# Kernel tuning notes

Measured on AMD Instinct MI355X. Metric: run time of the kernel, lower is better.

## Reference

```python
import jax, jax.numpy as jnp
import numpy as np

B, FEAT, HID, LAT, NQ, NEMB = 2048, 840, 256, 128, 12, 512


def setup_inputs() -> dict:
    key = jax.random.key(0)
    ks = jax.random.split(key, 6)
    return {
        "x": jax.random.normal(ks[0], (B, FEAT), jnp.float32),
        "w1": jax.random.normal(ks[1], (HID, 1, 3), jnp.float32) * 0.1,   # Conv1d(1->256, k=3)
        "b1": jnp.zeros((HID,), jnp.float32),
        "w2": jax.random.normal(ks[2], (LAT, HID, 3), jnp.float32) * 0.05,  # Conv1d(256->128, k=3)
        "b2": jnp.zeros((LAT,), jnp.float32),
        # 12 codebooks of (512, 128), init uniform(-1/n_emb, 1/n_emb) per the torch code
        "codebooks": jax.random.uniform(ks[3], (NQ, NEMB, LAT), jnp.float32, -1.0 / NEMB, 1.0 / NEMB),
    }


def _encode(x, w1, b1, w2, b2):
    # x: (B, FEAT) -> unsqueeze channel dim -> NCW conv stack -> adaptive avg pool(1)
    h = x[:, None, :]  # (B, 1, FEAT)
    h = jax.lax.conv_general_dilated(h, w1, (1,), 'SAME',
                                     dimension_numbers=('NCH', 'OIH', 'NCH'))
    h = jax.nn.relu(h + b1[None, :, None])
    h = jax.lax.conv_general_dilated(h, w2, (1,), 'SAME',
                                     dimension_numbers=('NCH', 'OIH', 'NCH'))
    h = jax.nn.relu(h + b2[None, :, None])
    return h.mean(axis=2)  # AdaptiveAvgPool1d(1) + squeeze -> (B, LAT)


def _rvq(z_flat, codebooks):
    # sequential residual VQ: 12 stages of cdist -> argmin -> gather -> residual update
    def step(residual, cb):
        # squared L2 distances: ||r||^2 - 2 r C^T + ||c||^2, shape (B, NEMB)
        d = (jnp.sum(residual ** 2, axis=1, keepdims=True)
             - 2.0 * (residual @ cb.T)
             + jnp.sum(cb ** 2, axis=1)[None, :])
        idx = jnp.argmin(d, axis=1)          # (B,)
        q = cb[idx]                          # (B, LAT) embedding gather
        residual = residual - jax.lax.stop_gradient(q)  # .detach() in torch
        return residual, (q, idx)

    _, (qs, idxs) = jax.lax.scan(step, z_flat, codebooks)  # qs: (NQ, B, LAT)
    return qs.sum(axis=0), idxs.T  # (B, LAT), (B, NQ)


def reference(x, w1, b1, w2, b2, codebooks):
    z = _encode(x, w1, b1, w2, b2)            # (B, LAT)
    zq, idx = _rvq(z, codebooks)              # L = 1 so flat == (B, LAT)
    return zq[:, None, :], idx[:, None, :]    # (B, 1, LAT), (B, 1, NQ)
```

## Files before the change

### kernel.cpp

```cpp
#include <hip/hip_runtime.h>

#define B_SZ 2048
#define FEAT 840
#define HID  256
#define LAT  128
#define NQ   12
#define NEMB 512

#define T_SUB 40
#define HSTR  43
#define H2STR 41

__device__ __forceinline__ float np8_combine(const float* r) {
    float sA = __fadd_rn(r[0], r[1]);
    float sB = __fadd_rn(r[2], r[3]);
    float sC = __fadd_rn(r[4], r[5]);
    float sD = __fadd_rn(r[6], r[7]);
    return __fadd_rn(__fadd_rn(sA, sB), __fadd_rn(sC, sD));
}

__global__ __launch_bounds__(256) void w2r_kernel(const float* __restrict__ w2,
                                                  float* __restrict__ w2r)
{
    int p = blockIdx.x * 256 + threadIdx.x;
    if (p >= HID * 384) return;
    int c2 = p / 384, r = p - c2 * 384;
    int ly = r / 12, jk = r - ly * 12;
    int j = jk / 3, k = jk - j * 3;
    w2r[p] = w2[(size_t)(ly*4 + j)*768 + c2*3 + k];
}

#define CSTEP(A0, A1, A2, H0, H1, H2, H3, H4, H5, H6)                  \
    {                                                                  \
        sk[0][0][0] = __fmaf_rn(A0.x, H0, sk[0][0][0]);                \
        sk[0][0][1] = __fmaf_rn(A0.y, H1, sk[0][0][1]);                \
        sk[0][0][2] = __fmaf_rn(A0.z, H2, sk[0][0][2]);                \
        sk[0][1][0] = __fmaf_rn(A0.x, H1, sk[0][1][0]);                \
        sk[0][1][1] = __fmaf_rn(A0.y, H2, sk[0][1][1]);                \
        sk[0][1][2] = __fmaf_rn(A0.z, H3, sk[0][1][2]);                \
        sk[0][2][0] = __fmaf_rn(A0.x, H2, sk[0][2][0]);                \
        sk[0][2][1] = __fmaf_rn(A0.y, H3, sk[0][2][1]);                \
        sk[0][2][2] = __fmaf_rn(A0.z, H4, sk[0][2][2]);                \
        sk[0][3][0] = __fmaf_rn(A0.x, H3, sk[0][3][0]);                \
        sk[0][3][1] = __fmaf_rn(A0.y, H4, sk[0][3][1]);                \
        sk[0][3][2] = __fmaf_rn(A0.z, H5, sk[0][3][2]);                \
        sk[0][4][0] = __fmaf_rn(A0.x, H4, sk[0][4][0]);                \
        sk[0][4][1] = __fmaf_rn(A0.y, H5, sk[0][4][1]);                \
        sk[0][4][2] = __fmaf_rn(A0.z, H6, sk[0][4][2]);                \
        sk[1][0][0] = __fmaf_rn(A0.w, H0, sk[1][0][0]);                \
        sk[1][0][1] = __fmaf_rn(A1.x, H1, sk[1][0][1]);                \
        sk[1][0][2] = __fmaf_rn(A1.y, H2, sk[1][0][2]);                \
        sk[1][1][0] = __fmaf_rn(A0.w, H1, sk[1][1][0]);                \
        sk[1][1][1] = __fmaf_rn(A1.x, H2, sk[1][1][1]);                \
        sk[1][1][2] = __fmaf_rn(A1.y, H3, sk[1][1][2]);                \
        sk[1][2][0] = __fmaf_rn(A0.w, H2, sk[1][2][0]);                \
        sk[1][2][1] = __fmaf_rn(A1.x, H3, sk[1][2][1]);                \
        sk[1][2][2] = __fmaf_rn(A1.y, H4, sk[1][2][2]);                \
        sk[1][3][0] = __fmaf_rn(A0.w, H3, sk[1][3][0]);                \
        sk[1][3][1] = __fmaf_rn(A1.x, H4, sk[1][3][1]);                \
        sk[1][3][2] = __fmaf_rn(A1.y, H5, sk[1][3][2]);                \
        sk[1][4][0] = __fmaf_rn(A0.w, H4, sk[1][4][0]);                \
        sk[1][4][1] = __fmaf_rn(A1.x, H5, sk[1][4][1]);                \
        sk[1][4][2] = __fmaf_rn(A1.y, H6, sk[1][4][2]);                \
        sk[2][0][0] = __fmaf_rn(A1.z, H0, sk[2][0][0]);                \
        sk[2][0][1] = __fmaf_rn(A1.w, H1, sk[2][0][1]);                \
        sk[2][0][2] = __fmaf_rn(A2.x, H2, sk[2][0][2]);                \
        sk[2][1][0] = __fmaf_rn(A1.z, H1, sk[2][1][0]);                \
        sk[2][1][1] = __fmaf_rn(A1.w, H2, sk[2][1][1]);                \
        sk[2][1][2] = __fmaf_rn(A2.x, H3, sk[2][1][2]);                \
        sk[2][2][0] = __fmaf_rn(A1.z, H2, sk[2][2][0]);                \
        sk[2][2][1] = __fmaf_rn(A1.w, H3, sk[2][2][1]);                \
        sk[2][2][2] = __fmaf_rn(A2.x, H4, sk[2][2][2]);                \
        sk[2][3][0] = __fmaf_rn(A1.z, H3, sk[2][3][0]);                \
        sk[2][3][1] = __fmaf_rn(A1.w, H4, sk[2][3][1]);                \
        sk[2][3][2] = __fmaf_rn(A2.x, H5, sk[2][3][2]);                \
        sk[2][4][0] = __fmaf_rn(A1.z, H4, sk[2][4][0]);                \
        sk[2][4][1] = __fmaf_rn(A1.w, H5, sk[2][4][1]);                \
        sk[2][4][2] = __fmaf_rn(A2.x, H6, sk[2][4][2]);                \
        sk[3][0][0] = __fmaf_rn(A2.y, H0, sk[3][0][0]);                \
        sk[3][0][1] = __fmaf_rn(A2.z, H1, sk[3][0][1]);                \
        sk[3][0][2] = __fmaf_rn(A2.w, H2, sk[3][0][2]);                \
        sk[3][1][0] = __fmaf_rn(A2.y, H1, sk[3][1][0]);                \
        sk[3][1][1] = __fmaf_rn(A2.z, H2, sk[3][1][1]);                \
        sk[3][1][2] = __fmaf_rn(A2.w, H3, sk[3][1][2]);                \
        sk[3][2][0] = __fmaf_rn(A2.y, H2, sk[3][2][0]);                \
        sk[3][2][1] = __fmaf_rn(A2.z, H3, sk[3][2][1]);                \
        sk[3][2][2] = __fmaf_rn(A2.w, H4, sk[3][2][2]);                \
        sk[3][3][0] = __fmaf_rn(A2.y, H3, sk[3][3][0]);                \
        sk[3][3][1] = __fmaf_rn(A2.z, H4, sk[3][3][1]);                \
        sk[3][3][2] = __fmaf_rn(A2.w, H5, sk[3][3][2]);                \
        sk[3][4][0] = __fmaf_rn(A2.y, H4, sk[3][4][0]);                \
        sk[3][4][1] = __fmaf_rn(A2.z, H5, sk[3][4][1]);                \
        sk[3][4][2] = __fmaf_rn(A2.w, H6, sk[3][4][2]);                \
    }

template <int USE_WR>
__global__ __launch_bounds__(256) void enc32_kernel(
    const float* __restrict__ x,  const float* __restrict__ w1,
    const float* __restrict__ b1, const float* __restrict__ w2,
    const float* __restrict__ w2r,
    const float* __restrict__ b2, float* __restrict__ zout)
{
    __shared__ float xp[FEAT + 4];
    __shared__ float h1s[HID * HSTR];
    __shared__ float leafs[LAT * 8];

    const int tid = threadIdx.x;
    const int b   = blockIdx.x;
    const int tx  = tid & 7;
    const int ly  = tid >> 3;
    const int u0  = tx * 5;

    const float wA = w1[tid*3+0], wB = w1[tid*3+1], wC = w1[tid*3+2];
    const float b1c = b1[tid];
    float b2v[4];
#pragma unroll
    for (int j = 0; j < 4; ++j) b2v[j] = b2[ly*4 + j];

    for (int i = tid; i < FEAT + 2; i += 256)
        xp[i] = (i >= 1 && i <= FEAT) ? x[(size_t)b*FEAT + i - 1] : 0.f;

    float racc[8];
    int leaf_id = 0, leaf_pos = 0;
#pragma unroll
    for (int j = 0; j < 8; ++j) racc[j] = 0.f;

    __syncthreads();
    for (int t0 = 0; t0 < FEAT; t0 += T_SUB) {
        const bool edge = (t0 == 0) | (t0 + T_SUB == FEAT);
        if (edge) {
            for (int tp = 0; tp < T_SUB + 2; ++tp) {
                int tg = t0 - 1 + tp;
                float v = 0.f;
                if (tg >= 0 && tg < FEAT) {
                    float s = __fadd_rn(__fadd_rn(__fmul_rn(wA, xp[tg]),
                                                  __fmul_rn(wB, xp[tg+1])),
                                        __fmul_rn(wC, xp[tg+2]));
                    s = __fadd_rn(s, b1c);
                    v = s > 0.f ? s : 0.f;
                }
                h1s[tid*HSTR + tp] = v;
            }
        } else {
#pragma unroll 2
            for (int tp = 0; tp < T_SUB + 2; ++tp) {
                int tg = t0 - 1 + tp;
                float s = __fadd_rn(__fadd_rn(__fmul_rn(wA, xp[tg]),
                                              __fmul_rn(wB, xp[tg+1])),
                                    __fmul_rn(wC, xp[tg+2]));
                s = __fadd_rn(s, b1c);
                h1s[tid*HSTR + tp] = s > 0.f ? s : 0.f;
            }
        }
        __syncthreads();

        float sk[4][5][3];
#pragma unroll
        for (int j = 0; j < 4; ++j)
#pragma unroll
            for (int i = 0; i < 5; ++i)
#pragma unroll
                for (int k = 0; k < 3; ++k) sk[j][i][k] = 0.f;

        if (USE_WR) {
            const float* __restrict__ wbase = w2r + ly*12;
            const float* __restrict__ hbase = &h1s[u0];

            float4 cA0, cA1, cA2, cB0, cB1, cB2;
            float  hA0, hA1, hA2, hA3, hA4, hA5, hA6;
            float  hB0, hB1, hB2, hB3, hB4, hB5, hB6;

            {
                const float4* pa = (const float4*)(wbase);
                const float4* pb = (const float4*)(wbase + 384);
                cA0 = pa[0]; cA1 = pa[1]; cA2 = pa[2];
                cB0 = pb[0]; cB1 = pb[1]; cB2 = pb[2];
                hA0 = hbase[0]; hA1 = hbase[1]; hA2 = hbase[2];
                hA3 = hbase[3]; hA4 = hbase[4]; hA5 = hbase[5]; hA6 = hbase[6];
                const float* hbB = hbase + HSTR;
                hB0 = hbB[0]; hB1 = hbB[1]; hB2 = hbB[2];
                hB3 = hbB[3]; hB4 = hbB[4]; hB5 = hbB[5]; hB6 = hbB[6];
            }

#pragma unroll 2
            for (int p = 0; p < HID/2 - 1; ++p) {
                const float* wn = wbase + (size_t)(p + 1) * 768;
                const float4* pa = (const float4*)(wn);
                const float4* pb = (const float4*)(wn + 384);
                float4 nA0 = pa[0], nA1 = pa[1], nA2 = pa[2];
                float4 nB0 = pb[0], nB1 = pb[1], nB2 = pb[2];
                const float* hn = hbase + (size_t)(p + 1) * 2 * HSTR;
                float nhA0 = hn[0], nhA1 = hn[1], nhA2 = hn[2], nhA3 = hn[3],
                      nhA4 = hn[4], nhA5 = hn[5], nhA6 = hn[6];
                const float* hnB = hn + HSTR;
                float nhB0 = hnB[0], nhB1 = hnB[1], nhB2 = hnB[2], nhB3 = hnB[3],
                      nhB4 = hnB[4], nhB5 = hnB[5], nhB6 = hnB[6];

                CSTEP(cA0, cA1, cA2, hA0, hA1, hA2, hA3, hA4, hA5, hA6)
                CSTEP(cB0, cB1, cB2, hB0, hB1, hB2, hB3, hB4, hB5, hB6)

                cA0 = nA0; cA1 = nA1; cA2 = nA2;
                cB0 = nB0; cB1 = nB1; cB2 = nB2;
                hA0 = nhA0; hA1 = nhA1; hA2 = nhA2; hA3 = nhA3;
                hA4 = nhA4; hA5 = nhA5; hA6 = nhA6;
                hB0 = nhB0; hB1 = nhB1; hB2 = nhB2; hB3 = nhB3;
                hB4 = nhB4; hB5 = nhB5; hB6 = nhB6;
            }
            CSTEP(cA0, cA1, cA2, hA0, hA1, hA2, hA3, hA4, hA5, hA6)
            CSTEP(cB0, cB1, cB2, hB0, hB1, hB2, hB3, hB4, hB5, hB6)
        } else {
            const float* __restrict__ wp = w2 + (size_t)(ly*4)*768;
            for (int c2 = 0; c2 < HID; ++c2) {
                const float* hp = &h1s[c2*HSTR + u0];
                float hv[7];
#pragma unroll
                for (int m = 0; m < 7; ++m) hv[m] = hp[m];
#pragma unroll
                for (int j = 0; j < 4; ++j) {
                    float wa = wp[j*768 + c2*3 + 0];
                    float wb = wp[j*768 + c2*3 + 1];
                    float wc = wp[j*768 + c2*3 + 2];
#pragma unroll
                    for (int i = 0; i < 5; ++i) {
                        sk[j][i][0] = __fmaf_rn(wa, hv[i],   sk[j][i][0]);
                        sk[j][i][1] = __fmaf_rn(wb, hv[i+1], sk[j][i][1]);
                        sk[j][i][2] = __fmaf_rn(wc, hv[i+2], sk[j][i][2]);
                    }
                }
            }
        }
        __syncthreads();

#pragma unroll
        for (int j = 0; j < 4; ++j)
#pragma unroll
            for (int i = 0; i < 5; ++i) {
                float hh = __fadd_rn(__fadd_rn(sk[j][i][0], sk[j][i][1]), sk[j][i][2]);
                hh = __fadd_rn(hh, b2v[j]);
                hh = hh > 0.f ? hh : 0.f;
                h1s[(ly*4 + j)*H2STR + u0 + i] = hh;
            }
        __syncthreads();

        if (tid < LAT) {
            for (int tt = 0; tt < T_SUB; ++tt) {
                float v = h1s[tid*H2STR + tt];
                int j = leaf_pos & 7;
                racc[j] = (leaf_pos < 8) ? v : __fadd_rn(racc[j], v);
                ++leaf_pos;
                int llen = (leaf_id == 7) ? 112 : 104;
                if (leaf_pos == llen) {
                    leafs[tid*8 + leaf_id] = np8_combine(racc);
                    ++leaf_id; leaf_pos = 0;
                }
            }
        }
        __syncthreads();
    }

    if (tid < LAT) {
        const float* L = &leafs[tid*8];
        float s0 = __fadd_rn(L[0], L[1]);
        float s1 = __fadd_rn(L[2], L[3]);
        float sA = __fadd_rn(s0, s1);
        float s2 = __fadd_rn(L[4], L[5]);
        float s3 = __fadd_rn(L[6], L[7]);
        float sB = __fadd_rn(s2, s3);
        float tot = __fadd_rn(sA, sB);
        zout[(size_t)b*LAT + tid] = __fdiv_rn(tot, 840.0f);
    }
}

__global__ __launch_bounds__(256) void rvq32_kernel(
    const float* __restrict__ cb, const float* __restrict__ z,
    float* __restrict__ zqout, float* __restrict__ oidx)
{
    __shared__ float rr[LAT];
    __shared__ float Ash;
    __shared__ float redd[256];
    __shared__ int   rede[256];
    __shared__ float sredd[64];
    __shared__ int   srede[64];
    __shared__ int   beste;
    __shared__ float qv[NQ * LAT];

    const int tid = threadIdx.x;
    const int b   = blockIdx.x;

    if (tid < LAT) rr[tid] = z[(size_t)b*LAT + tid];
    __syncthreads();

    for (int q = 0; q < NQ; ++q) {
        const float* __restrict__ cbq = cb + (size_t)q * NEMB * LAT;

        if (tid == 0) {
            float r8[8];
#pragma unroll
            for (int j = 0; j < 8; ++j) r8[j] = __fmul_rn(rr[j], rr[j]);
            for (int i = 8; i < LAT; i += 8)
#pragma unroll
                for (int j = 0; j < 8; ++j)
                    r8[j] = __fadd_rn(r8[j], __fmul_rn(rr[i+j], rr[i+j]));
            Ash = np8_combine(r8);
        }
        __syncthreads();

        float dmin = 0.f; int emin = 0;
#pragma unroll
        for (int h = 0; h < 2; ++h) {
            int e = 2*tid + h;
            const float* __restrict__ cp = cbq + (size_t)e*LAT;
            float dot = 0.f;
            float c8[8];
#pragma unroll
            for (int j = 0; j < 8; ++j) {
                float c = cp[j];
                c8[j] = __fmul_rn(c, c);
                dot = __fmaf_rn(c, rr[j], dot);
            }
            for (int i = 8; i < LAT; i += 8)
#pragma unroll
                for (int j = 0; j < 8; ++j) {
                    float c = cp[i+j];
                    dot = __fmaf_rn(c, rr[i+j], dot);
                    c8[j] = __fadd_rn(c8[j], __fmul_rn(c, c));
                }
            float cn = np8_combine(c8);
            float G  = __fmul_rn(2.0f, dot);
            float d  = __fadd_rn(__fsub_rn(Ash, G), cn);
            if (h == 0) { dmin = d; emin = e; }
            else if (d < dmin) { dmin = d; emin = e; }
        }
        redd[tid] = dmin; rede[tid] = emin;
        __syncthreads();

        if (tid < 64) {
            float bb = redd[tid*4]; int ee = rede[tid*4];
            for (int j = 1; j < 4; ++j) {
                float dj = redd[tid*4 + j];
                if (dj < bb) { bb = dj; ee = rede[tid*4 + j]; }
            }
            sredd[tid] = bb; srede[tid] = ee;
        }
        __syncthreads();
        if (tid == 0) {
            float bb = sredd[0]; int ee = srede[0];
            for (int j = 1; j < 64; ++j) {
                float dj = sredd[j];
                if (dj < bb) { bb = dj; ee = srede[j]; }
            }
            beste = ee;
            oidx[(size_t)b*NQ + q] = (float)ee;
        }
        __syncthreads();

        if (tid < LAT) {
            float cv = cbq[(size_t)beste*LAT + tid];
            qv[q*LAT + tid] = cv;
            rr[tid] = __fsub_rn(rr[tid], cv);
        }
        __syncthreads();
    }

    if (tid < LAT) {
        float s = qv[tid];
        for (int s2 = 1; s2 < NQ; ++s2)
            s = __fadd_rn(s, qv[s2*LAT + tid]);
        zqout[(size_t)b*LAT + tid] = s;
    }
}

extern "C" void kernel_launch(void* const* d_in, const int* in_sizes, int n_in,
                              void* d_out, int out_size, void* d_ws, size_t ws_size,
                              hipStream_t stream)
{
    (void)in_sizes; (void)n_in; (void)out_size;
    const float* x  = (const float*)d_in[0];
    const float* w1 = (const float*)d_in[1];
    const float* b1 = (const float*)d_in[2];
    const float* w2 = (const float*)d_in[3];
    const float* b2 = (const float*)d_in[4];
    const float* cb = (const float*)d_in[5];

    float* out  = (float*)d_out;
    float* zq   = out;
    float* oidx = out + (size_t)B_SZ * LAT;

    const size_t w2r_bytes = (size_t)HID * 384 * sizeof(float);

    if (ws_size >= w2r_bytes) {
        float* w2r = (float*)d_ws;
        w2r_kernel<<<(HID*384 + 255)/256, 256, 0, stream>>>(w2, w2r);
        enc32_kernel<1><<<B_SZ, 256, 0, stream>>>(x, w1, b1, w2, w2r, b2, zq);
    } else {
        enc32_kernel<0><<<B_SZ, 256, 0, stream>>>(x, w1, b1, w2, nullptr, b2, zq);
    }
    rvq32_kernel<<<B_SZ, 256, 0, stream>>>(cb, zq, zq, oidx);
}
```

Before: 6.231 ms.

## Transpose conv1 activations in LDS and repack w2 into 4-channel chunks

The conv1 output tile in shared memory changes from channel-major with stride 43 to time-major with stride 260, so each thread can read four input channels at once with float4 loads. The w2 repack kernel now groups weights in chunks of 4 input channels per output-row group, and the inner loop handles 4 channels per iteration with 12 float4 weight loads and 7 float4 activation loads. This removes the scalar LDS loads and the manual software prefetch of the previous loop. In exchange it raises register pressure, and the conv1 writes now land at stride 260 with possible bank conflicts.

Measured after the change: 6.553 ms. +5.2%, slower.

```diff
diff --git a/kernel.cpp b/kernel.cpp
--- a/kernel.cpp
+++ b/kernel.cpp
@@ -8,7 +8,8 @@
 #define NEMB 512
 
 #define T_SUB 40
-#define HSTR  43
+#define NU    42
+#define HTSTR 260
 #define H2STR 41
 
 __device__ __forceinline__ float np8_combine(const float* r) {
@@ -19,15 +20,17 @@
     return __fadd_rn(__fadd_rn(sA, sB), __fadd_rn(sC, sD));
 }
 
-__global__ __launch_bounds__(256) void w2r_kernel(const float* __restrict__ w2,
-                                                  float* __restrict__ w2r)
+__global__ __launch_bounds__(256) void w2q_kernel(const float* __restrict__ w2,
+                                                  float* __restrict__ w2q)
 {
-    int p = blockIdx.x * 256 + threadIdx.x;
-    if (p >= HID * 384) return;
-    int c2 = p / 384, r = p - c2 * 384;
-    int ly = r / 12, jk = r - ly * 12;
-    int j = jk / 3, k = jk - j * 3;
-    w2r[p] = w2[(size_t)(ly*4 + j)*768 + c2*3 + k];
+    int o = blockIdx.x * 256 + threadIdx.x;
+    if (o >= HID * 384) return;
+    int ch  = o / 1536, rem = o - ch * 1536;
+    int ly  = rem / 48, s48 = rem - ly * 48;
+    int q   = s48 / 12, jk  = s48 - q * 12;
+    int j   = jk / 3,   k   = jk - j * 3;
+    int c2  = ch * 4 + q;
+    w2q[o] = w2[(size_t)(ly*4 + j)*768 + c2*3 + k];
 }
 
 #define CSTEP(A0, A1, A2, H0, H1, H2, H3, H4, H5, H6)                  \
@@ -94,15 +97,15 @@
         sk[3][4][2] = __fmaf_rn(A2.w, H6, sk[3][4][2]);                \
     }
 
-template <int USE_WR>
+template <int USE_WQ>
 __global__ __launch_bounds__(256) void enc32_kernel(
     const float* __restrict__ x,  const float* __restrict__ w1,
     const float* __restrict__ b1, const float* __restrict__ w2,
-    const float* __restrict__ w2r,
+    const float* __restrict__ w2q,
     const float* __restrict__ b2, float* __restrict__ zout)
 {
     __shared__ float xp[FEAT + 4];
-    __shared__ float h1s[HID * HSTR];
+    __shared__ float h1t[NU * HTSTR];
     __shared__ float leafs[LAT * 8];
 
     const int tid = threadIdx.x;
@@ -128,9 +131,10 @@
     __syncthreads();
     for (int t0 = 0; t0 < FEAT; t0 += T_SUB) {
         const bool edge = (t0 == 0) | (t0 + T_SUB == FEAT);
+        float* hw = &h1t[tid];
         if (edge) {
-            for (int tp = 0; tp < T_SUB + 2; ++tp) {
-                int tg = t0 - 1 + tp;
+            for (int u = 0; u < NU; ++u) {
+                int tg = t0 - 1 + u;
                 float v = 0.f;
                 if (tg >= 0 && tg < FEAT) {
                     float s = __fadd_rn(__fadd_rn(__fmul_rn(wA, xp[tg]),
@@ -139,17 +143,17 @@
                     s = __fadd_rn(s, b1c);
                     v = s > 0.f ? s : 0.f;
                 }
-                h1s[tid*HSTR + tp] = v;
+                hw[u*HTSTR] = v;
             }
         } else {
 #pragma unroll 2
-            for (int tp = 0; tp < T_SUB + 2; ++tp) {
-                int tg = t0 - 1 + tp;
+            for (int u = 0; u < NU; ++u) {
+                int tg = t0 - 1 + u;
                 float s = __fadd_rn(__fadd_rn(__fmul_rn(wA, xp[tg]),
                                               __fmul_rn(wB, xp[tg+1])),
                                     __fmul_rn(wC, xp[tg+2]));
                 s = __fadd_rn(s, b1c);
-                h1s[tid*HSTR + tp] = s > 0.f ? s : 0.f;
+                hw[u*HTSTR] = s > 0.f ? s : 0.f;
             }
         }
         __syncthreads();
@@ -162,59 +166,36 @@
 #pragma unroll
                 for (int k = 0; k < 3; ++k) sk[j][i][k] = 0.f;
 
-        if (USE_WR) {
-            const float* __restrict__ wbase = w2r + ly*12;
-            const float* __restrict__ hbase = &h1s[u0];
-
-            float4 cA0, cA1, cA2, cB0, cB1, cB2;
-            float  hA0, hA1, hA2, hA3, hA4, hA5, hA6;
-            float  hB0, hB1, hB2, hB3, hB4, hB5, hB6;
-
-            {
-                const float4* pa = (const float4*)(wbase);
-                const float4* pb = (const float4*)(wbase + 384);
-                cA0 = pa[0]; cA1 = pa[1]; cA2 = pa[2];
-                cB0 = pb[0]; cB1 = pb[1]; cB2 = pb[2];
-                hA0 = hbase[0]; hA1 = hbase[1]; hA2 = hbase[2];
-                hA3 = hbase[3]; hA4 = hbase[4]; hA5 = hbase[5]; hA6 = hbase[6];
-                const float* hbB = hbase + HSTR;
-                hB0 = hbB[0]; hB1 = hbB[1]; hB2 = hbB[2];
-                hB3 = hbB[3]; hB4 = hbB[4]; hB5 = hbB[5]; hB6 = hbB[6];
-            }
-
+        if (USE_WQ) {
+            const float* __restrict__ hb = &h1t[u0 * HTSTR];
 #pragma unroll 2
-            for (int p = 0; p < HID/2 - 1; ++p) {
-                const float* wn = wbase + (size_t)(p + 1) * 768;
-                const float4* pa = (const float4*)(wn);
-                const float4* pb = (const float4*)(wn + 384);
-                float4 nA0 = pa[0], nA1 = pa[1], nA2 = pa[2];
-                float4 nB0 = pb[0], nB1 = pb[1], nB2 = pb[2];
-                const float* hn = hbase + (size_t)(p + 1) * 2 * HSTR;
-                float nhA0 = hn[0], nhA1 = hn[1], nhA2 = hn[2], nhA3 = hn[3],
-                      nhA4 = hn[4], nhA5 = hn[5], nhA6 = hn[6];
-                const float* hnB = hn + HSTR;
-                float nhB0 = hnB[0], nhB1 = hnB[1], nhB2 = hnB[2], nhB3 = hnB[3],
-                      nhB4 = hnB[4], nhB5 = hnB[5], nhB6 = hnB[6];
-
-                CSTEP(cA0, cA1, cA2, hA0, hA1, hA2, hA3, hA4, hA5, hA6)
-                CSTEP(cB0, cB1, cB2, hB0, hB1, hB2, hB3, hB4, hB5, hB6)
-
-                cA0 = nA0; cA1 = nA1; cA2 = nA2;
-                cB0 = nB0; cB1 = nB1; cB2 = nB2;
-                hA0 = nhA0; hA1 = nhA1; hA2 = nhA2; hA3 = nhA3;
-                hA4 = nhA4; hA5 = nhA5; hA6 = nhA6;
-                hB0 = nhB0; hB1 = nhB1; hB2 = nhB2; hB3 = nhB3;
-                hB4 = nhB4; hB5 = nhB5; hB6 = nhB6;
-            }
-            CSTEP(cA0, cA1, cA2, hA0, hA1, hA2, hA3, hA4, hA5, hA6)
-            CSTEP(cB0, cB1, cB2, hB0, hB1, hB2, hB3, hB4, hB5, hB6)
+            for (int ch = 0; ch < HID/4; ++ch) {
+                const float4* wq = (const float4*)(w2q + ((size_t)ch*32 + ly)*48);
+                float4 q0 = wq[0],  q1 = wq[1],  q2 = wq[2];
+                float4 q3 = wq[3],  q4 = wq[4],  q5 = wq[5];
+                float4 q6 = wq[6],  q7 = wq[7],  q8 = wq[8];
+                float4 q9 = wq[9],  q10 = wq[10], q11 = wq[11];
+                const float4* h0p = (const float4*)(hb + 0*HTSTR + ch*4);
+                const float4* h1p = (const float4*)(hb + 1*HTSTR + ch*4);
+                const float4* h2p = (const float4*)(hb + 2*HTSTR + ch*4);
+                const float4* h3p = (const float4*)(hb + 3*HTSTR + ch*4);
+                const float4* h4p = (const float4*)(hb + 4*HTSTR + ch*4);
+                const float4* h5p = (const float4*)(hb + 5*HTSTR + ch*4);
+                const float4* h6p = (const float4*)(hb + 6*HTSTR + ch*4);
+                float4 m0 = *h0p, m1 = *h1p, m2 = *h2p, m3 = *h3p;
+                float4 m4 = *h4p, m5 = *h5p, m6 = *h6p;
+                CSTEP(q0, q1, q2,  m0.x, m1.x, m2.x, m3.x, m4.x, m5.x, m6.x)
+                CSTEP(q3, q4, q5,  m0.y, m1.y, m2.y, m3.y, m4.y, m5.y, m6.y)
+                CSTEP(q6, q7, q8,  m0.z, m1.z, m2.z, m3.z, m4.z, m5.z, m6.z)
+                CSTEP(q9, q10, q11, m0.w, m1.w, m2.w, m3.w, m4.w, m5.w, m6.w)
+            }
         } else {
             const float* __restrict__ wp = w2 + (size_t)(ly*4)*768;
+            const float* __restrict__ hb = &h1t[u0 * HTSTR];
             for (int c2 = 0; c2 < HID; ++c2) {
-                const float* hp = &h1s[c2*HSTR + u0];
                 float hv[7];
 #pragma unroll
-                for (int m = 0; m < 7; ++m) hv[m] = hp[m];
+                for (int m = 0; m < 7; ++m) hv[m] = hb[m*HTSTR + c2];
 #pragma unroll
                 for (int j = 0; j < 4; ++j) {
                     float wa = wp[j*768 + c2*3 + 0];
@@ -238,13 +219,13 @@
                 float hh = __fadd_rn(__fadd_rn(sk[j][i][0], sk[j][i][1]), sk[j][i][2]);
                 hh = __fadd_rn(hh, b2v[j]);
                 hh = hh > 0.f ? hh : 0.f;
-                h1s[(ly*4 + j)*H2STR + u0 + i] = hh;
+                h1t[(ly*4 + j)*H2STR + u0 + i] = hh;
             }
         __syncthreads();
 
         if (tid < LAT) {
             for (int tt = 0; tt < T_SUB; ++tt) {
-                float v = h1s[tid*H2STR + tt];
+                float v = h1t[tid*H2STR + tt];
                 int j = leaf_pos & 7;
                 racc[j] = (leaf_pos < 8) ? v : __fadd_rn(racc[j], v);
                 ++leaf_pos;
@@ -386,12 +367,12 @@
     float* zq   = out;
     float* oidx = out + (size_t)B_SZ * LAT;
 
-    const size_t w2r_bytes = (size_t)HID * 384 * sizeof(float);
-
-    if (ws_size >= w2r_bytes) {
-        float* w2r = (float*)d_ws;
-        w2r_kernel<<<(HID*384 + 255)/256, 256, 0, stream>>>(w2, w2r);
-        enc32_kernel<1><<<B_SZ, 256, 0, stream>>>(x, w1, b1, w2, w2r, b2, zq);
+    const size_t w2q_bytes = (size_t)HID * 384 * sizeof(float);
+
+    if (ws_size >= w2q_bytes) {
+        float* w2q = (float*)d_ws;
+        w2q_kernel<<<(HID*384 + 255)/256, 256, 0, stream>>>(w2, w2q);
+        enc32_kernel<1><<<B_SZ, 256, 0, stream>>>(x, w1, b1, w2, w2q, b2, zq);
     } else {
         enc32_kernel<0><<<B_SZ, 256, 0, stream>>>(x, w1, b1, w2, nullptr, b2, zq);
     }
```
